# Kernel optimization log

Hardware: AMD Instinct MI355X
Metric: run time of the kernel (lower is better)

Reference implementation:

```python
import jax, jax.numpy as jnp
import numpy as np

TOP_K = 3
COMMIT = 0.25


def setup_inputs() -> dict:
    key = jax.random.key(0)
    k1, k2, k3 = jax.random.split(key, 3)
    features = jax.random.normal(k1, (197, 128, 768), dtype=jnp.float32)
    class_emb = jax.random.normal(k2, (4096, 768), dtype=jnp.float32)
    feat_emb = jax.random.normal(k3, (4096, 768), dtype=jnp.float32)
    return {"features": features, "class_emb": class_emb, "feat_emb": feat_emb}


def _vq(x, emb):
    # x: [A, B, C]; emb: [K, C]
    A, B, C = x.shape
    K = emb.shape[0]
    N = A * B
    flat = x.reshape(N, C)
    d = (jnp.sum(flat * flat, axis=1, keepdims=True)
         + jnp.sum(emb * emb, axis=1)
         - 2.0 * flat @ emb.T)                      # [N, K]
    _, idx = jax.lax.top_k(-d, TOP_K)               # smallest-k indices [N, k]
    quant = emb[idx].reshape(A, B, TOP_K, C)        # gather codewords
    xr = x[:, :, None, :]                           # [A, B, 1, C]
    e_latent_loss = jnp.mean((jax.lax.stop_gradient(quant) - jnp.broadcast_to(xr, quant.shape)) ** 2)
    loss = COMMIT * e_latent_loss
    q_st = xr + jax.lax.stop_gradient(quant - xr)   # straight-through [A,B,k,C]
    # avg_probs: mean over rows of the top-k one-hot encodings (rows sum to k)
    counts = jnp.zeros((K,), x.dtype).at[idx.reshape(-1)].add(1.0)
    avg_probs = counts / N
    perplexity = jnp.exp(-jnp.sum(avg_probs * jnp.log(avg_probs + 1e-10)))
    return loss, q_st, perplexity, avg_probs, idx.reshape(A, B, TOP_K), d.reshape(A, B, K)


def _forward(features, class_emb, feat_emb):
    cl_loss, cl_q, cl_perp, cl_avg, cl_idx, cl_dist = _vq(features[0:1], class_emb)
    ft_loss, ft_q, ft_perp, ft_avg, ft_idx, ft_dist = _vq(features[1:], feat_emb)
    Kc = class_emb.shape[0]
    Kf = feat_emb.shape[0]
    FMAX = jnp.float32(np.finfo(np.float32).max)
    B = features.shape[1]
    T = features.shape[0] - 1
    cl_dist_p = jnp.concatenate([cl_dist, jnp.full((1, B, Kf), FMAX, jnp.float32)], axis=-1)
    ft_dist_p = jnp.concatenate([jnp.full((T, B, Kc), FMAX, jnp.float32), ft_dist], axis=-1)
    distances = jnp.concatenate([cl_dist_p, ft_dist_p], axis=0)          # [T+1, B, Kc+Kf]
    encoding_indices = jnp.concatenate([cl_idx, ft_idx + Kc], axis=0)    # [T+1, B, k]
    quantized = jnp.concatenate([cl_q, ft_q], axis=0)                    # [T+1, B, k, C]
    loss = ft_loss + cl_loss
    return (loss, quantized, cl_perp, ft_perp, cl_avg, ft_avg, encoding_indices, distances)


def reference(features, class_emb, feat_emb):
    return _forward(features, class_emb, feat_emb)
```

## Files before the change

### kernel.cpp

```cpp
#include <hip/hip_runtime.h>
#include <math.h>

#define DEVFN __device__ __forceinline__

typedef short  s16x8 __attribute__((ext_vector_type(8)));
typedef float  f32x4 __attribute__((ext_vector_type(4)));

constexpr int C     = 768;
constexpr int NROWS = 25216;
constexpr int NCL   = 128;
constexpr int KCB   = 4096;
constexpr int KOUT  = 8192;
constexpr int TK    = 3;
constexpr int NT    = 24;
constexpr int MT    = 197;
constexpr int NTB   = 16;

constexpr long long QUANT_OFF  = 1;
constexpr long long QUANT_SZ   = (long long)NROWS * TK * C;
constexpr long long CLPERP_OFF = QUANT_OFF + QUANT_SZ;
constexpr long long FTPERP_OFF = CLPERP_OFF + 1;
constexpr long long CLAVG_OFF  = FTPERP_OFF + 1;
constexpr long long FTAVG_OFF  = CLAVG_OFF + KCB;
constexpr long long ENC_OFF    = FTAVG_OFF + KCB;
constexpr long long DIST_OFF   = ENC_OFF + (long long)NROWS * TK;

constexpr size_t XS_ELE = (size_t)MT * NT * 4096;
constexpr size_t ES_ELE = (size_t)2 * NTB * NT * 8192;

constexpr float FMAXV = 3.4028234663852886e38f;
constexpr float PADV  = 3.3895313892515355e38f;

DEVFN void gload_lds16(const void* g, void* l) {
    __builtin_amdgcn_global_load_lds(
        (const __attribute__((address_space(1))) unsigned*)g,
        (__attribute__((address_space(3))) unsigned*)l, 16, 0, 0);
}

DEVFN bool better(float v, int i, float bv, int bi) {
    return (v < bv) | ((v == bv) & (i < bi));
}
DEVFN void ins3(float v, int i, float& v0, int& i0, float& v1, int& i1, float& v2, int& i2) {
    const bool b0 = better(v, i, v0, i0);
    const bool b1 = better(v, i, v1, i1);
    const bool b2 = better(v, i, v2, i2);
    const float nv1 = b0 ? v0 : (b1 ? v : v1);
    const int   ni1 = b0 ? i0 : (b1 ? i : i1);
    const float nv2 = b1 ? v1 : (b2 ? v : v2);
    const int   ni2 = b1 ? i1 : (b2 ? i : i2);
    v0 = b0 ? v : v0;  i0 = b0 ? i : i0;
    v1 = nv1;          i1 = ni1;
    v2 = nv2;          i2 = ni2;
}

__global__ void init_kernel(float* counts) {
    int i = blockIdx.x * blockDim.x + threadIdx.x;
    if (i < KOUT) counts[i] = 0.0f;
}

__global__ void norms_kernel(const float* __restrict__ X,
                             const float* __restrict__ CE,
                             const float* __restrict__ FE,
                             float* __restrict__ xnorm,
                             float* __restrict__ enorm) {
    int row  = blockIdx.x * 4 + (threadIdx.x >> 6);
    int lane = threadIdx.x & 63;
    const int TOT = NROWS + 2 * KCB;
    if (row >= TOT) return;
    const float* src; float* dst;
    if (row < NROWS) { src = X + (long long)row * C; dst = xnorm + row; }
    else {
        int r = row - NROWS;
        src = (r < KCB) ? (CE + (long long)r * C) : (FE + (long long)(r - KCB) * C);
        dst = enorm + r;
    }
    const float4* p = (const float4*)src;
    float s = 0.f;
    for (int j = lane; j < C / 4; j += 64) {
        float4 v = p[j];
        s += v.x*v.x + v.y*v.y + v.z*v.z + v.w*v.w;
    }
    for (int o = 32; o > 0; o >>= 1) s += __shfl_down(s, o);
    if (lane == 0) *dst = s;
}

__global__ __launch_bounds__(256)
void presplit_kernel(const float* __restrict__ X,
                     const float* __restrict__ CE,
                     const float* __restrict__ FE,
                     short* __restrict__ XsH, short* __restrict__ XsL,
                     short* __restrict__ EsH, short* __restrict__ EsL) {
    const int b = blockIdx.x;
    const float* src; char* dH; char* dL; int nrr;
    if (b < MT * NT) {
        const int tile = b / NT, ks = b % NT;
        src = X + (size_t)tile * 128 * C + ks * 32;
        dH = (char*)(XsH + (size_t)b * 4096);
        dL = (char*)(XsL + (size_t)b * 4096);
        nrr = 2;
    } else {
        const int bb = b - MT * NT;
        const int book = bb / (NTB * NT);
        const int rem  = bb % (NTB * NT);
        const int tile = rem / NT, ks = rem % NT;
        src = (book ? FE : CE) + (size_t)tile * 256 * C + ks * 32;
        dH = (char*)(EsH + (size_t)bb * 8192);
        dL = (char*)(EsL + (size_t)bb * 8192);
        nrr = 4;
    }
    const int tid = threadIdx.x;
    const int row = tid >> 2, oc = tid & 3;
    for (int rr = 0; rr < nrr; ++rr) {
        const int r = row + rr * 64;
        const float* s = src + (size_t)r * C + oc * 8;
        float4 v0 = *(const float4*)s;
        float4 v1 = *(const float4*)(s + 4);
        float f[8] = {v0.x, v0.y, v0.z, v0.w, v1.x, v1.y, v1.z, v1.w};
        s16x8 hi, lo;
        #pragma unroll
        for (int q = 0; q < 8; ++q) {
            unsigned u = __float_as_uint(f[q]);
            hi[q] = (short)(u >> 16);
            lo[q] = (short)(__float_as_uint(f[q] - __uint_as_float(u & 0xffff0000u)) >> 16);
        }
        const int off = (r * 64 + oc * 16) ^ ((r & 7) << 4);
        *(s16x8*)(dH + off) = hi;
        *(s16x8*)(dL + off) = lo;
    }
}

__global__ __launch_bounds__(512, 2)
void gemm_dist_kernel(const short* __restrict__ XsH, const short* __restrict__ XsL,
                      const short* __restrict__ EsH, const short* __restrict__ EsL,
                      const float* __restrict__ xnorm,
                      const float* __restrict__ enorm,
                      float* __restrict__ dist) {
    __shared__ __align__(16) char smem[3 * 49152];

    const int orig = blockIdx.y * gridDim.x + blockIdx.x;
    const int wg   = (orig & 7) * 394 + (orig >> 3);
    const int mt = wg >> 4, nt = wg & 15;

    const int m0 = mt * 128, n0 = nt * 256;
    const int colbase = (mt == 0) ? 0 : KCB;
    const int btile = ((mt == 0) ? 0 : NTB) + nt;
    const int tid = threadIdx.x, l = tid & 63, w = tid >> 6;
    const int wy = w >> 2, wx = w & 3;

    const char* sbase[6]; size_t sstr[6]; int ldso[6];
    #pragma unroll
    for (int i = 0; i < 6; ++i) {
        const int wc = w * 6 + i;
        const char* pb; int within; size_t st;
        if (wc < 8)       { pb = (const char*)XsH + (size_t)mt * NT * 8192;     within = wc * 1024;        st = 8192;  }
        else if (wc < 16) { pb = (const char*)XsL + (size_t)mt * NT * 8192;     within = (wc - 8) * 1024;  st = 8192;  }
        else if (wc < 32) { pb = (const char*)EsH + (size_t)btile * NT * 16384; within = (wc - 16) * 1024; st = 16384; }
        else              { pb = (const char*)EsL + (size_t)btile * NT * 16384; within = (wc - 32) * 1024; st = 16384; }
        sbase[i] = pb + within + l * 16;
        sstr[i]  = st;
        ldso[i]  = wc * 1024 + l * 16;
    }
    auto STAGE = [&](int buf, int t) {
        #pragma unroll
        for (int i = 0; i < 6; ++i)
            gload_lds16(sbase[i] + (size_t)t * sstr[i], smem + buf * 49152 + ldso[i]);
    };

    const int arow = wy * 64 + (l & 15);
    const int brow = wx * 64 + (l & 15);
    const int abase = (arow * 64 + ((l >> 4) * 16)) ^ ((l & 7) << 4);
    const int bbase = (brow * 64 + ((l >> 4) * 16)) ^ ((l & 7) << 4);

    f32x4 acc[4][4];
    #pragma unroll
    for (int i = 0; i < 4; ++i)
        #pragma unroll
        for (int j = 0; j < 4; ++j) acc[i][j] = (f32x4){0.f, 0.f, 0.f, 0.f};

    STAGE(0, 0);
    STAGE(1, 1);
    int cur = 0;
    for (int t = 0; t < NT; ++t) {
        if (t + 2 < NT) STAGE((cur + 2 >= 3) ? cur - 1 : cur + 2, t + 2);

        if (t + 2 < NT)      { asm volatile("s_waitcnt vmcnt(12)" ::: "memory"); }
        else if (t + 1 < NT) { asm volatile("s_waitcnt vmcnt(6)"  ::: "memory"); }
        else                 { asm volatile("s_waitcnt vmcnt(0)"  ::: "memory"); }
        __builtin_amdgcn_s_barrier();
        __builtin_amdgcn_sched_barrier(0);

        const char* sb = smem + cur * 49152;
        s16x8 ah[4], bh[4];
        #pragma unroll
        for (int i = 0; i < 4; ++i) ah[i] = *(const s16x8*)(sb + abase + i * 1024);
        #pragma unroll
        for (int j = 0; j < 4; ++j) bh[j] = *(const s16x8*)(sb + 16384 + bbase + j * 1024);
        #pragma unroll
        for (int i = 0; i < 4; ++i)
            #pragma unroll
            for (int j = 0; j < 4; ++j)
                acc[i][j] = __builtin_amdgcn_mfma_f32_16x16x32_bf16(ah[i], bh[j], acc[i][j], 0, 0, 0);

        s16x8 al[4];
        #pragma unroll
        for (int i = 0; i < 4; ++i) al[i] = *(const s16x8*)(sb + 8192 + abase + i * 1024);
        #pragma unroll
        for (int i = 0; i < 4; ++i)
            #pragma unroll
            for (int j = 0; j < 4; ++j)
                acc[i][j] = __builtin_amdgcn_mfma_f32_16x16x32_bf16(al[i], bh[j], acc[i][j], 0, 0, 0);

        s16x8 bl[4];
        #pragma unroll
        for (int j = 0; j < 4; ++j) bl[j] = *(const s16x8*)(sb + 32768 + bbase + j * 1024);
        #pragma unroll
        for (int i = 0; i < 4; ++i)
            #pragma unroll
            for (int j = 0; j < 4; ++j)
                acc[i][j] = __builtin_amdgcn_mfma_f32_16x16x32_bf16(ah[i], bl[j], acc[i][j], 0, 0, 0);

        __builtin_amdgcn_sched_barrier(0);
        asm volatile("s_waitcnt lgkmcnt(0)" ::: "memory");
        __builtin_amdgcn_s_barrier();
        cur = (cur == 2) ? 0 : cur + 1;
    }

    const int lr = (l >> 4) * 4;
    const int lc = l & 15;
    float en_r[4];
    #pragma unroll
    for (int j = 0; j < 4; ++j) en_r[j] = enorm[colbase + n0 + wx * 64 + j * 16 + lc];
    #pragma unroll
    for (int i = 0; i < 4; ++i) {
        #pragma unroll
        for (int q = 0; q < 4; ++q) {
            const int gm = m0 + wy * 64 + i * 16 + lr + q;
            const float xnv = xnorm[gm];
            float* o = dist + (long long)gm * KOUT + colbase + n0 + wx * 64 + lc;
            #pragma unroll
            for (int j = 0; j < 4; ++j)
                o[j * 16] = (xnv + en_r[j]) - 2.0f * acc[i][j][q];
        }
    }

    const int padbase = (mt == 0) ? KCB : 0;
    for (int r2 = w; r2 < 128; r2 += 8) {
        float* p = dist + (long long)(m0 + r2) * KOUT + padbase + n0;
        p[l] = PADV; p[l + 64] = PADV; p[l + 128] = PADV; p[l + 192] = PADV;
    }
}

__global__ __launch_bounds__(256, 4)
void topk_kernel(const float* __restrict__ dist,
                 int* __restrict__ idxbuf,
                 float* __restrict__ out,
                 float* __restrict__ counts) {
    int rb = blockIdx.x * 4 + (threadIdx.x >> 6);
    if (rb >= NROWS) return;
    const int row = NROWS - 1 - rb;
    const int lane = threadIdx.x & 63;
    const int colbase = (row < NCL) ? 0 : KCB;
    const float* d = dist + (long long)row * KOUT + colbase;
    float v0 = FMAXV, v1 = FMAXV, v2 = FMAXV;
    int   i0 = 0x7fffffff, i1 = 0x7fffffff, i2 = 0x7fffffff;

    const float4* dv = (const float4*)(d + 1);

    float4 b[16];
    #pragma unroll
    for (int it = 0; it < 15; ++it) b[it] = dv[it * 64 + lane];
    const bool hasLast = (960 + lane) < 1023;
    b[15] = hasLast ? dv[960 + lane]
                    : (float4){FMAXV, FMAXV, FMAXV, FMAXV};
    #pragma unroll
    for (int it = 0; it < 15; ++it) {
        const int k = 1 + (it * 64 + lane) * 4;
        ins3(b[it].x, k,     v0, i0, v1, i1, v2, i2);
        ins3(b[it].y, k + 1, v0, i0, v1, i1, v2, i2);
        ins3(b[it].z, k + 2, v0, i0, v1, i1, v2, i2);
        ins3(b[it].w, k + 3, v0, i0, v1, i1, v2, i2);
    }
    {
        const int k = 1 + (960 + lane) * 4;
        const int kk = hasLast ? k : 0x7ffffff0;
        ins3(b[15].x, kk,     v0, i0, v1, i1, v2, i2);
        ins3(b[15].y, kk + 1, v0, i0, v1, i1, v2, i2);
        ins3(b[15].z, kk + 2, v0, i0, v1, i1, v2, i2);
        ins3(b[15].w, kk + 3, v0, i0, v1, i1, v2, i2);
    }
    if (lane < 4) {
        const int k = (lane == 0) ? 0 : 4092 + lane;
        ins3(d[k], k, v0, i0, v1, i1, v2, i2);
    }

    #pragma unroll
    for (int off = 32; off > 0; off >>= 1) {
        float w0 = __shfl_down(v0, off), w1 = __shfl_down(v1, off), w2 = __shfl_down(v2, off);
        int   j0 = __shfl_down(i0, off), j1 = __shfl_down(i1, off), j2 = __shfl_down(i2, off);
        ins3(w0, j0, v0, i0, v1, i1, v2, i2);
        ins3(w1, j1, v0, i0, v1, i1, v2, i2);
        ins3(w2, j2, v0, i0, v1, i1, v2, i2);
    }
    if (lane == 0) {
        long long rt = (long long)row * TK;
        idxbuf[rt + 0] = i0; idxbuf[rt + 1] = i1; idxbuf[rt + 2] = i2;
        out[ENC_OFF + rt + 0] = (float)(i0 + colbase);
        out[ENC_OFF + rt + 1] = (float)(i1 + colbase);
        out[ENC_OFF + rt + 2] = (float)(i2 + colbase);
        atomicAdd(&counts[i0 + colbase], 1.0f);
        atomicAdd(&counts[i1 + colbase], 1.0f);
        atomicAdd(&counts[i2 + colbase], 1.0f);
    }
}

__global__ __launch_bounds__(192)
void gather_kernel(const float* __restrict__ X,
                   const float* __restrict__ CE,
                   const float* __restrict__ FE,
                   const int* __restrict__ idxbuf,
                   float* __restrict__ out,
                   float* __restrict__ partials) {
    const int row = blockIdx.x;
    const int tid = threadIdx.x;
    const float4 xv = ((const float4*)(X + (size_t)row * C))[tid];
    const float* Ebase = (row < NCL) ? CE : FE;
    const long long rt0 = (long long)row * TK;
    float s = 0.f;
    #pragma unroll
    for (int t = 0; t < TK; ++t) {
        const int id = idxbuf[rt0 + t];
        const float4 ev = ((const float4*)(Ebase + (size_t)id * C))[tid];
        const float d0 = ev.x - xv.x, d1 = ev.y - xv.y, d2 = ev.z - xv.z, d3 = ev.w - xv.w;
        s += d0*d0 + d1*d1 + d2*d2 + d3*d3;
        float* q = out + QUANT_OFF + (rt0 + t) * C + tid * 4;
        q[0] = xv.x + d0; q[1] = xv.y + d1; q[2] = xv.z + d2; q[3] = xv.w + d3;
    }
    #pragma unroll
    for (int o = 32; o > 0; o >>= 1) s += __shfl_down(s, o);
    __shared__ float red[3];
    const int lane = tid & 63, w = tid >> 6;
    if (lane == 0) red[w] = s;
    __syncthreads();
    if (tid == 0) partials[row] = red[0] + red[1] + red[2];
}

__global__ void finalize_kernel(const float* __restrict__ counts,
                                const float* __restrict__ partials,
                                float* __restrict__ out) {
    __shared__ float  red[2][4];
    __shared__ double redd[2][4];
    int tid = threadIdx.x, lane = tid & 63, w = tid >> 6;
    float ecl = 0.f, eft = 0.f;
    for (int i = tid; i < KCB; i += blockDim.x) {
        float p = counts[i] * (1.0f / 128.0f);
        out[CLAVG_OFF + i] = p;
        ecl += p * logf(p + 1e-10f);
        float qv = counts[KCB + i] * (1.0f / 25088.0f);
        out[FTAVG_OFF + i] = qv;
        eft += qv * logf(qv + 1e-10f);
    }
    double scl = 0.0, sft = 0.0;
    for (int i = tid; i < NROWS; i += blockDim.x) {
        double v = (double)partials[i];
        if (i < NCL) scl += v; else sft += v;
    }
    for (int o = 32; o > 0; o >>= 1) {
        ecl += __shfl_down(ecl, o); eft += __shfl_down(eft, o);
        scl += __shfl_down(scl, o); sft += __shfl_down(sft, o);
    }
    if (lane == 0) { red[0][w] = ecl; red[1][w] = eft; redd[0][w] = scl; redd[1][w] = sft; }
    __syncthreads();
    if (tid == 0) {
        float tcl = red[0][0] + red[0][1] + red[0][2] + red[0][3];
        float tft = red[1][0] + red[1][1] + red[1][2] + red[1][3];
        double dcl = redd[0][0] + redd[0][1] + redd[0][2] + redd[0][3];
        double dft = redd[1][0] + redd[1][1] + redd[1][2] + redd[1][3];
        out[CLPERP_OFF] = expf(-tcl);
        out[FTPERP_OFF] = expf(-tft);
        float cl_loss = 0.25f * (float)(dcl / 294912.0);
        float ft_loss = 0.25f * (float)(dft / 57802752.0);
        out[0] = ft_loss + cl_loss;
    }
}

extern "C" void kernel_launch(void* const* d_in, const int* in_sizes, int n_in,
                              void* d_out, int out_size, void* d_ws, size_t ws_size,
                              hipStream_t stream) {
    const float* X  = (const float*)d_in[0];
    const float* CE = (const float*)d_in[1];
    const float* FE = (const float*)d_in[2];
    float* out = (float*)d_out;

    float* ws_f   = (float*)d_ws;
    float* xnorm  = ws_f;
    float* enorm  = ws_f + NROWS;
    float* counts = ws_f + NROWS + KOUT;
    int*   idxbuf = (int*)(ws_f + NROWS + 2 * KOUT);
    float* ssepart = xnorm;
    float* dist   = out + DIST_OFF;

    short* XsH = (short*)(out + 4);
    short* XsL = XsH + XS_ELE;
    short* EsH = XsL + XS_ELE;
    short* EsL = EsH + ES_ELE;

    init_kernel<<<32, 256, 0, stream>>>(counts);
    norms_kernel<<<(NROWS + 2 * KCB) / 4, 256, 0, stream>>>(X, CE, FE, xnorm, enorm);
    presplit_kernel<<<MT * NT + 2 * NTB * NT, 256, 0, stream>>>(X, CE, FE, XsH, XsL, EsH, EsL);
    gemm_dist_kernel<<<dim3(NTB, MT), 512, 0, stream>>>(XsH, XsL, EsH, EsL, xnorm, enorm, dist);
    topk_kernel<<<NROWS / 4, 256, 0, stream>>>(dist, idxbuf, out, counts);
    gather_kernel<<<NROWS, 192, 0, stream>>>(X, CE, FE, idxbuf, out, ssepart);
    finalize_kernel<<<1, 256, 0, stream>>>(counts, ssepart, out);
}
```

Before: 1.773 ms.

## Interleave prefetch loads with MFMA phases and raise wave priority during MFMA

The three-stage LDS pipeline now issues the global-to-LDS prefetch for tile t+2 in three pairs, one per MFMA phase, instead of all six loads at the start of the iteration. Each phase waits on its LDS reads and is wrapped in s_setprio so MFMA work gets issue priority, with a barrier between phases. The aim is to spread memory issue across compute and keep the matrix units busy. The cost is two extra workgroup barriers per iteration, and the vmcnt wait now depends on the previous iteration's loads having completed.

```diff
diff --git a/kernel.cpp b/kernel.cpp
--- a/kernel.cpp
+++ b/kernel.cpp
@@ -160,10 +160,16 @@
         sstr[i]  = st;
         ldso[i]  = wc * 1024 + l * 16;
     }
-    auto STAGE = [&](int buf, int t) {
+    auto STAGE_ALL = [&](int buf, int t) {
         #pragma unroll
         for (int i = 0; i < 6; ++i)
             gload_lds16(sbase[i] + (size_t)t * sstr[i], smem + buf * 49152 + ldso[i]);
+    };
+    auto STAGE_PAIR = [&](int buf, int t, int p) {
+        #pragma unroll
+        for (int i = 0; i < 2; ++i)
+            gload_lds16(sbase[p * 2 + i] + (size_t)t * sstr[p * 2 + i],
+                        smem + buf * 49152 + ldso[p * 2 + i]);
     };
 
     const int arow = wy * 64 + (l & 15);
@@ -177,51 +183,66 @@
         #pragma unroll
         for (int j = 0; j < 4; ++j) acc[i][j] = (f32x4){0.f, 0.f, 0.f, 0.f};
 
-    STAGE(0, 0);
-    STAGE(1, 1);
+    STAGE_ALL(0, 0);
+    STAGE_ALL(1, 1);
     int cur = 0;
     for (int t = 0; t < NT; ++t) {
-        if (t + 2 < NT) STAGE((cur + 2 >= 3) ? cur - 1 : cur + 2, t + 2);
-
-        if (t + 2 < NT)      { asm volatile("s_waitcnt vmcnt(12)" ::: "memory"); }
-        else if (t + 1 < NT) { asm volatile("s_waitcnt vmcnt(6)"  ::: "memory"); }
-        else                 { asm volatile("s_waitcnt vmcnt(0)"  ::: "memory"); }
+        const int nbuf = (cur + 2 >= 3) ? cur - 1 : cur + 2;
+        const bool pf = (t + 2 < NT);
+
+        if (t + 1 < NT) { asm volatile("s_waitcnt vmcnt(6)" ::: "memory"); }
+        else            { asm volatile("s_waitcnt vmcnt(0)" ::: "memory"); }
         __builtin_amdgcn_s_barrier();
+
+        const char* sb = smem + cur * 49152;
+
+        s16x8 ah[4], bh[4];
+        #pragma unroll
+        for (int i = 0; i < 4; ++i) ah[i] = *(const s16x8*)(sb + abase + i * 1024);
+        #pragma unroll
+        for (int j = 0; j < 4; ++j) bh[j] = *(const s16x8*)(sb + 16384 + bbase + j * 1024);
+        if (pf) STAGE_PAIR(nbuf, t + 2, 0);
+        asm volatile("s_waitcnt lgkmcnt(0)" ::: "memory");
         __builtin_amdgcn_sched_barrier(0);
-
-        const char* sb = smem + cur * 49152;
-        s16x8 ah[4], bh[4];
-        #pragma unroll
-        for (int i = 0; i < 4; ++i) ah[i] = *(const s16x8*)(sb + abase + i * 1024);
-        #pragma unroll
-        for (int j = 0; j < 4; ++j) bh[j] = *(const s16x8*)(sb + 16384 + bbase + j * 1024);
+        __builtin_amdgcn_s_setprio(1);
         #pragma unroll
         for (int i = 0; i < 4; ++i)
             #pragma unroll
             for (int j = 0; j < 4; ++j)
                 acc[i][j] = __builtin_amdgcn_mfma_f32_16x16x32_bf16(ah[i], bh[j], acc[i][j], 0, 0, 0);
+        __builtin_amdgcn_s_setprio(0);
+        __builtin_amdgcn_s_barrier();
 
         s16x8 al[4];
         #pragma unroll
         for (int i = 0; i < 4; ++i) al[i] = *(const s16x8*)(sb + 8192 + abase + i * 1024);
+        if (pf) STAGE_PAIR(nbuf, t + 2, 1);
+        asm volatile("s_waitcnt lgkmcnt(0)" ::: "memory");
+        __builtin_amdgcn_sched_barrier(0);
+        __builtin_amdgcn_s_setprio(1);
         #pragma unroll
         for (int i = 0; i < 4; ++i)
             #pragma unroll
             for (int j = 0; j < 4; ++j)
                 acc[i][j] = __builtin_amdgcn_mfma_f32_16x16x32_bf16(al[i], bh[j], acc[i][j], 0, 0, 0);
+        __builtin_amdgcn_s_setprio(0);
+        __builtin_amdgcn_s_barrier();
 
         s16x8 bl[4];
         #pragma unroll
         for (int j = 0; j < 4; ++j) bl[j] = *(const s16x8*)(sb + 32768 + bbase + j * 1024);
+        if (pf) STAGE_PAIR(nbuf, t + 2, 2);
+        asm volatile("s_waitcnt lgkmcnt(0)" ::: "memory");
+        __builtin_amdgcn_sched_barrier(0);
+        __builtin_amdgcn_s_setprio(1);
         #pragma unroll
         for (int i = 0; i < 4; ++i)
             #pragma unroll
             for (int j = 0; j < 4; ++j)
                 acc[i][j] = __builtin_amdgcn_mfma_f32_16x16x32_bf16(ah[i], bl[j], acc[i][j], 0, 0, 0);
-
-        __builtin_amdgcn_sched_barrier(0);
-        asm volatile("s_waitcnt lgkmcnt(0)" ::: "memory");
+        __builtin_amdgcn_s_setprio(0);
         __builtin_amdgcn_s_barrier();
+
         cur = (cur == 2) ? 0 : cur + 1;
     }
 
```

Measured after the change: 1.712 ms, median of 2. 3.4% less time.
